# Kernel optimization log

Hardware: AMD Instinct MI355X
Metric: run time of the kernel (lower is better)

Reference implementation:

```python
import jax, jax.numpy as jnp
import numpy as np
import math

N = 8
METHOD = 'low0'


def _dct_matrix(n):
    A = np.zeros((n, n), dtype=np.float32)
    A[0, :] = math.sqrt(1.0 / n)
    for i in range(1, n):
        for j in range(n):
            A[i, j] = math.cos(math.pi * i * (2 * j + 1) / (2 * n)) * math.sqrt(2.0 / n)
    return A


def _freq_mask(n, method):
    if 'low' in method:
        num_freq = int(method[3:])
        ax = [0, 0, 1, 2, 1, 0, 0, 1, 2, 3, 4, 3, 2, 1, 0, 0, 1, 2, 3, 4, 5]
        ay = [0, 1, 0, 0, 1, 2, 3, 2, 1, 0, 0, 1, 2, 3, 4, 5, 4, 3, 2, 1, 0]
        mx = [t * (n // 8) for t in ax[:num_freq + 1]]
        my = [t * (n // 8) for t in ay[:num_freq + 1]]
    else:
        mx, my = [0], [0]
    m = np.zeros((n, n), dtype=np.float32)
    m[np.array(mx), np.array(my)] = 1.0
    return m


def setup_inputs() -> dict:
    key = jax.random.key(0)
    x = jax.random.normal(key, (8, 32, 512, 512), dtype=jnp.float32)
    A = jnp.asarray(_dct_matrix(N))
    mask = jnp.asarray(_freq_mask(N, METHOD))
    return {"x": x, "A": A, "mask": mask}


def _block_split(x, n_blk):
    # (n,c,h,w) -> (n, wb*hb*c, N, N); matches split(h)->cat(c), split(w)->cat(c)
    n, c, h, w = x.shape
    hb, wb = h // n_blk, w // n_blk
    x = x.reshape(n, c, hb, n_blk, wb, n_blk)
    x = x.transpose(0, 4, 2, 1, 3, 5)  # (n, wb, hb, c, N, N)
    return x.reshape(n, wb * hb * c, n_blk, n_blk)


def _block_merge(xb, n, c, hb, wb, n_blk):
    # inverse of _block_split
    xb = xb.reshape(n, wb, hb, c, n_blk, n_blk)
    xb = xb.transpose(0, 3, 2, 4, 1, 5)  # (n, c, hb, N, wb, N)
    return xb.reshape(n, c, hb * n_blk, wb * n_blk)


def reference(x, A, mask):
    n, c, h, w = x.shape
    n_blk = A.shape[0]
    hb, wb = h // n_blk, w // n_blk
    x4 = _block_split(x, n_blk)                       # (n, wb*hb*c, N, N)
    fre = jnp.einsum('jk,nckl->ncjl', A, x4)          # A @ x
    fre = jnp.einsum('ncjk,lk->ncjl', fre, A)         # ... @ A^T  -> 2D DCT
    fre_low = fre * mask                              # keep selected freqs only
    xl = jnp.einsum('kj,nckl->ncjl', A, fre_low)      # A^T @ fre_low
    xl = jnp.einsum('ncjk,kl->ncjl', xl, A)           # ... @ A    -> inverse DCT
    x_low = _block_merge(xl, n, c, hb, wb, n_blk)
    x_high = x - x_low
    return (x_low, x_high)
```

## Files before the change

### kernel.cpp

```cpp
#include <hip/hip_runtime.h>


typedef float f32x4 __attribute__((ext_vector_type(4)));

#define IMG_W 512u
#define HALF_ELEMS 67108864u

__global__ __launch_bounds__(256) void dct_lowpass_kernel(
    const float* __restrict__ x,
    const float* __restrict__ A,
    const float* __restrict__ mask,
    float* __restrict__ xlow,
    float* __restrict__ xhigh)
{
    const unsigned gid = blockIdx.x * 256u + threadIdx.x;
    const unsigned nc  = gid >> 12;
    const unsigned rem = gid & 4095u;
    const unsigned bh  = rem >> 6;
    const unsigned bw  = rem & 63u;
    const size_t base = ((size_t)nc * 512u + bh * 8u) * 512u + bw * 8u;

    float X[8][8];
#pragma unroll
    for (int r = 0; r < 8; ++r) {
        const f32x4* p = reinterpret_cast<const f32x4*>(x + base + (size_t)r * IMG_W);
        f32x4 a = __builtin_nontemporal_load(p);
        f32x4 b = __builtin_nontemporal_load(p + 1);
        X[r][0] = a.x; X[r][1] = a.y; X[r][2] = a.z; X[r][3] = a.w;
        X[r][4] = b.x; X[r][5] = b.y; X[r][6] = b.z; X[r][7] = b.w;
    }

    float L[8][8];
#pragma unroll
    for (int j = 0; j < 8; ++j)
#pragma unroll
        for (int l = 0; l < 8; ++l) L[j][l] = 0.f;

#pragma unroll
    for (int i = 0; i < 8; ++i) {
#pragma unroll
        for (int k = 0; k < 8; ++k) {
            const float m = mask[i * 8 + k];
            if (m != 0.0f) {
                float c = 0.f;
#pragma unroll
                for (int j = 0; j < 8; ++j) {
                    float r = 0.f;
#pragma unroll
                    for (int l = 0; l < 8; ++l) r = fmaf(X[j][l], A[k * 8 + l], r);
                    c = fmaf(A[i * 8 + j], r, c);
                }
                c *= m;
#pragma unroll
                for (int j = 0; j < 8; ++j) {
                    const float cj = c * A[i * 8 + j];
#pragma unroll
                    for (int l = 0; l < 8; ++l)
                        L[j][l] = fmaf(cj, A[k * 8 + l], L[j][l]);
                }
            }
        }
    }

#pragma unroll
    for (int r = 0; r < 8; ++r) {
        f32x4 lo0 = { L[r][0], L[r][1], L[r][2], L[r][3] };
        f32x4 lo1 = { L[r][4], L[r][5], L[r][6], L[r][7] };
        f32x4 hi0 = { X[r][0] - L[r][0], X[r][1] - L[r][1],
                      X[r][2] - L[r][2], X[r][3] - L[r][3] };
        f32x4 hi1 = { X[r][4] - L[r][4], X[r][5] - L[r][5],
                      X[r][6] - L[r][6], X[r][7] - L[r][7] };
        f32x4* pl = reinterpret_cast<f32x4*>(xlow + base + (size_t)r * IMG_W);
        f32x4* ph = reinterpret_cast<f32x4*>(xhigh + base + (size_t)r * IMG_W);
        __builtin_nontemporal_store(lo0, pl);
        __builtin_nontemporal_store(lo1, pl + 1);
        __builtin_nontemporal_store(hi0, ph);
        __builtin_nontemporal_store(hi1, ph + 1);
    }
}

extern "C" void kernel_launch(void* const* d_in, const int* in_sizes, int n_in,
                              void* d_out, int out_size, void* d_ws, size_t ws_size,
                              hipStream_t stream) {
    const float* x    = (const float*)d_in[0];
    const float* A    = (const float*)d_in[1];
    const float* mask = (const float*)d_in[2];
    float* xlow  = (float*)d_out;
    float* xhigh = (float*)d_out + HALF_ELEMS;

    dim3 grid(4096);
    dim3 block(256);
    hipLaunchKernelGGL(dct_lowpass_kernel, grid, block, 0, stream,
                       x, A, mask, xlow, xhigh);
}
```

Before: 736.9 us.

## Split each 8x8 DCT block across two lanes with shuffle reduction

Each 8x8 block is now handled by two adjacent threads, each owning a 4-column half. The partial DCT coefficient is combined with a lane shuffle, and the grid doubles to 8192 blocks. This halves per-thread registers and gives adjacent lanes contiguous 16-byte accesses, which should coalesce memory traffic better and raise occupancy (launch bounds now request 4 blocks). Nontemporal loads and stores are replaced with plain vector accesses, which may change cache behaviour for this streaming kernel.

```diff
diff --git a/kernel.cpp b/kernel.cpp
--- a/kernel.cpp
+++ b/kernel.cpp
@@ -3,38 +3,35 @@
 
 typedef float f32x4 __attribute__((ext_vector_type(4)));
 
-#define IMG_W 512u
 #define HALF_ELEMS 67108864u
 
-__global__ __launch_bounds__(256) void dct_lowpass_kernel(
+__global__ __launch_bounds__(256, 4) void dct_lowpass_kernel(
     const float* __restrict__ x,
     const float* __restrict__ A,
     const float* __restrict__ mask,
     float* __restrict__ xlow,
     float* __restrict__ xhigh)
 {
-    const unsigned gid = blockIdx.x * 256u + threadIdx.x;
-    const unsigned nc  = gid >> 12;
-    const unsigned rem = gid & 4095u;
-    const unsigned bh  = rem >> 6;
-    const unsigned bw  = rem & 63u;
-    const size_t base = ((size_t)nc * 512u + bh * 8u) * 512u + bw * 8u;
+    const unsigned T   = blockIdx.x * 256u + threadIdx.x;
+    const unsigned nc  = T >> 13;
+    const unsigned rem = T & 8191u;
+    const unsigned bh  = rem >> 7;
+    const unsigned wi  = rem & 127u;
+    const unsigned half = T & 1u;
+    const size_t rowbase = ((size_t)nc * 512u + bh * 8u) * 512u + wi * 4u;
 
-    float X[8][8];
+    float X[8][4];
 #pragma unroll
     for (int r = 0; r < 8; ++r) {
-        const f32x4* p = reinterpret_cast<const f32x4*>(x + base + (size_t)r * IMG_W);
-        f32x4 a = __builtin_nontemporal_load(p);
-        f32x4 b = __builtin_nontemporal_load(p + 1);
-        X[r][0] = a.x; X[r][1] = a.y; X[r][2] = a.z; X[r][3] = a.w;
-        X[r][4] = b.x; X[r][5] = b.y; X[r][6] = b.z; X[r][7] = b.w;
+        f32x4 v = *reinterpret_cast<const f32x4*>(x + rowbase + (size_t)r * 512u);
+        X[r][0] = v.x; X[r][1] = v.y; X[r][2] = v.z; X[r][3] = v.w;
     }
 
-    float L[8][8];
+    float L[8][4];
 #pragma unroll
-    for (int j = 0; j < 8; ++j)
+    for (int r = 0; r < 8; ++r)
 #pragma unroll
-        for (int l = 0; l < 8; ++l) L[j][l] = 0.f;
+        for (int l = 0; l < 4; ++l) L[r][l] = 0.f;
 
 #pragma unroll
     for (int i = 0; i < 8; ++i) {
@@ -42,21 +39,27 @@
         for (int k = 0; k < 8; ++k) {
             const float m = mask[i * 8 + k];
             if (m != 0.0f) {
-                float c = 0.f;
+                float ak[4];
+#pragma unroll
+                for (int l = 0; l < 4; ++l)
+                    ak[l] = half ? A[k * 8 + 4 + l] : A[k * 8 + l];
+
+                float cp = 0.f;
 #pragma unroll
                 for (int j = 0; j < 8; ++j) {
-                    float r = 0.f;
+                    float rr = 0.f;
 #pragma unroll
-                    for (int l = 0; l < 8; ++l) r = fmaf(X[j][l], A[k * 8 + l], r);
-                    c = fmaf(A[i * 8 + j], r, c);
+                    for (int l = 0; l < 4; ++l) rr = fmaf(X[j][l], ak[l], rr);
+                    cp = fmaf(A[i * 8 + j], rr, cp);
                 }
-                c *= m;
+                const float c = (cp + __shfl_xor(cp, 1)) * m;
+
 #pragma unroll
-                for (int j = 0; j < 8; ++j) {
-                    const float cj = c * A[i * 8 + j];
+                for (int r = 0; r < 8; ++r) {
+                    const float cr = c * A[i * 8 + r];
 #pragma unroll
-                    for (int l = 0; l < 8; ++l)
-                        L[j][l] = fmaf(cj, A[k * 8 + l], L[j][l]);
+                    for (int l = 0; l < 4; ++l)
+                        L[r][l] = fmaf(cr, ak[l], L[r][l]);
                 }
             }
         }
@@ -64,18 +67,11 @@
 
 #pragma unroll
     for (int r = 0; r < 8; ++r) {
-        f32x4 lo0 = { L[r][0], L[r][1], L[r][2], L[r][3] };
-        f32x4 lo1 = { L[r][4], L[r][5], L[r][6], L[r][7] };
-        f32x4 hi0 = { X[r][0] - L[r][0], X[r][1] - L[r][1],
-                      X[r][2] - L[r][2], X[r][3] - L[r][3] };
-        f32x4 hi1 = { X[r][4] - L[r][4], X[r][5] - L[r][5],
-                      X[r][6] - L[r][6], X[r][7] - L[r][7] };
-        f32x4* pl = reinterpret_cast<f32x4*>(xlow + base + (size_t)r * IMG_W);
-        f32x4* ph = reinterpret_cast<f32x4*>(xhigh + base + (size_t)r * IMG_W);
-        __builtin_nontemporal_store(lo0, pl);
-        __builtin_nontemporal_store(lo1, pl + 1);
-        __builtin_nontemporal_store(hi0, ph);
-        __builtin_nontemporal_store(hi1, ph + 1);
+        f32x4 lo = { L[r][0], L[r][1], L[r][2], L[r][3] };
+        f32x4 hi = { X[r][0] - L[r][0], X[r][1] - L[r][1],
+                     X[r][2] - L[r][2], X[r][3] - L[r][3] };
+        *reinterpret_cast<f32x4*>(xlow  + rowbase + (size_t)r * 512u) = lo;
+        *reinterpret_cast<f32x4*>(xhigh + rowbase + (size_t)r * 512u) = hi;
     }
 }
 
@@ -88,7 +84,7 @@
     float* xlow  = (float*)d_out;
     float* xhigh = (float*)d_out + HALF_ELEMS;
 
-    dim3 grid(4096);
+    dim3 grid(8192);
     dim3 block(256);
     hipLaunchKernelGGL(dct_lowpass_kernel, grid, block, 0, stream,
                        x, A, mask, xlow, xhigh);
```

Result: faster. 692.6 us (-6.0%).
